# Kernel tuning notes

Hardware: AMD Instinct MI355X
Metric: run time of the kernel (lower is better)

Reference implementation:

```python
import jax, jax.numpy as jnp
import numpy as np

B = 8192          # batch
DEPTH = 2         # variational layers
NCLS = 10         # classes
WIRES = 4         # qubits -> 16-dim statevector
NPATCH = 196      # 14x14 patches of 2x2 on a 28x28 image

# Pauli-Z expectation table: row i = (+1/-1) per wire for basis state i (wire 0 = MSB)
_bits = (np.arange(16)[:, None] >> np.array([3, 2, 1, 0])) & 1
_ZTAB = jnp.asarray(1.0 - 2.0 * _bits, dtype=jnp.float32)  # (16, 4)


def _ry(state, ang, wire):
    # Apply RY(ang) (real rotation) on `wire`; state shape (N,2,2,2,2)
    c = jnp.cos(0.5 * ang)
    s = jnp.sin(0.5 * ang)
    a0 = jnp.take(state, 0, axis=wire + 1)
    a1 = jnp.take(state, 1, axis=wire + 1)
    return jnp.stack([c * a0 - s * a1, s * a0 + c * a1], axis=wire + 1)


def _cnot01(state):  # control wire 0 (axis 1), target wire 1 (axis 2)
    return jnp.stack([state[:, 0], state[:, 1, ::-1]], axis=1)


def _cnot23(state):  # control wire 2 (axis 3), target wire 3 (axis 4)
    return jnp.stack([state[:, :, :, 0], state[:, :, :, 1, ::-1]], axis=3)


def _quanv(patches, theta):
    # patches: (N, 4) pixel angles. Batched 4-qubit statevector simulation.
    half = 0.5 * patches
    v = jnp.stack([jnp.cos(half), jnp.sin(half)], axis=-1)  # (N,4,2): RY(x_w)|0>
    state = jnp.einsum('na,nb,nc,nd->nabcd', v[:, 0], v[:, 1], v[:, 2], v[:, 3])
    for d in range(theta.shape[0]):
        for w in range(WIRES):
            state = _ry(state, theta[d, w], w)
        state = _cnot01(state)
        state = _cnot23(state)
    probs = (state * state).reshape(state.shape[0], 16)
    return probs @ _ZTAB  # (N, 4) <Z_w> expectations


def setup_inputs() -> dict:
    key = jax.random.key(0)
    k1, k2, k3 = jax.random.split(key, 3)
    x = jax.random.normal(k1, (B, 1, 28, 28), dtype=jnp.float32)
    theta = jax.random.normal(k2, (DEPTH, WIRES), dtype=jnp.float32)
    W = jax.random.normal(k3, (NCLS, NPATCH * WIRES), dtype=jnp.float32) * 0.03
    b = jnp.zeros((NCLS,), dtype=jnp.float32)
    return {"x": x, "theta": theta, "W": W, "b": b}


def reference(x, theta, W, b):
    bsz = x.shape[0]
    # extract 2x2 patches in (row-block, col-block) order, pixels row-major
    patches = (x[:, 0]
               .reshape(bsz, 14, 2, 14, 2)
               .transpose(0, 1, 3, 2, 4)
               .reshape(bsz * NPATCH, 4))
    qfeat = _quanv(patches, theta).reshape(bsz, NPATCH * WIRES)  # (B, 784)
    logits = qfeat @ W.T + b
    return jax.nn.log_softmax(logits, axis=-1)
```

## Files before the change

### kernel.cpp

```cpp
#include <hip/hip_runtime.h>
#include <math.h>

#define NP 196
#define NC 10


template<int CTRL>
__device__ __forceinline__ float dpp_add(float v) {
    int t = __builtin_amdgcn_update_dpp(0, __float_as_int(v), CTRL, 0xF, 0xF, true);
    return v + __int_as_float(t);
}

__device__ __forceinline__ float swz_xor16_add(float v) {
    int t = __builtin_amdgcn_ds_swizzle(__float_as_int(v), 0x401F);
    return v + __int_as_float(t);
}

__device__ __forceinline__ void sim_pair(float pxa, float pxb,
                                         float th0a, float th0b,
                                         float ct0, float st0,
                                         float ct1, float st1,
                                         float& z0, float& z1) {
    float sa, ca, sb, cb;
    __sincosf(0.5f * (pxa + th0a), &sa, &ca);
    __sincosf(0.5f * (pxb + th0b), &sb, &cb);
    float p0 = ca * cb, p1 = ca * sb, p2 = sa * sb, p3 = sa * cb;
    float q0 = ct0 * p0 - st0 * p2, q2 = st0 * p0 + ct0 * p2;
    float q1 = ct0 * p1 - st0 * p3, q3 = st0 * p1 + ct0 * p3;
    float r0 = ct1 * q0 - st1 * q1, r1 = st1 * q0 + ct1 * q1;
    float r2 = ct1 * q2 - st1 * q3, r3 = st1 * q2 + ct1 * q3;
    float e0 = r0 * r0, e1 = r1 * r1, e2 = r2 * r2, e3 = r3 * r3;
    z0 = (e0 + e1) - (e2 + e3);
    z1 = (e0 - e1) + (e3 - e2);
}

__global__ __launch_bounds__(256, 2) void quanv_fused(
    const float* __restrict__ x,
    const float* __restrict__ theta,
    const float* __restrict__ W,
    const float* __restrict__ bias,
    float* __restrict__ out,
    int B)
{
    const int tid  = threadIdx.x;
    const int lane = tid & 63;
    const int wave = blockIdx.x * 4 + (tid >> 6);
    const int imgbase = wave * 4;
    if (imgbase >= B) return;

    const float th00 = theta[0], th01 = theta[1], th02 = theta[2], th03 = theta[3];
    float ct[4], st[4];
#pragma unroll
    for (int w = 0; w < 4; ++w) __sincosf(0.5f * theta[4 + w], &st[w], &ct[w]);

    const float* x0 = x + (size_t)imgbase * 784;

    float acc[4][NC];
#pragma unroll
    for (int m = 0; m < 4; ++m)
#pragma unroll
        for (int c = 0; c < NC; ++c) acc[m][c] = 0.f;

#pragma unroll
    for (int k = 0; k < 4; ++k) {
        const bool active = (k < 3) || (lane < 4);
        const int p = lane + 64 * k;
        const int pi = p / 14;
        const int pj = p - pi * 14;
        const int off = pi * 56 + pj * 2;

        float f[4][4];
        if (active) {
#pragma unroll
            for (int m = 0; m < 4; ++m) {
                const float* xm = x0 + m * 784 + off;
                const float2 r0 = *(const float2*)(xm);
                const float2 r1 = *(const float2*)(xm + 28);
                sim_pair(r0.x, r0.y, th00, th01, ct[0], st[0], ct[1], st[1],
                         f[m][0], f[m][1]);
                sim_pair(r1.x, r1.y, th02, th03, ct[2], st[2], ct[3], st[3],
                         f[m][2], f[m][3]);
            }
#pragma unroll
            for (int c = 0; c < NC; ++c) {
                const float4 w4 = *(const float4*)(W + c * 784 + p * 4);
#pragma unroll
                for (int m = 0; m < 4; ++m) {
                    acc[m][c] = fmaf(f[m][0], w4.x, fmaf(f[m][1], w4.y,
                                fmaf(f[m][2], w4.z, fmaf(f[m][3], w4.w, acc[m][c]))));
                }
            }
        }
    }

    const bool lo32 = (lane & 32) == 0;
    const bool lo16 = (lane & 16) == 0;
    float m4[NC];
#pragma unroll
    for (int c = 0; c < NC; ++c) {
        float tAB = lo32 ? acc[0][c] : acc[1][c];
        float uAB = lo32 ? acc[1][c] : acc[0][c];
        float mAB = tAB + __shfl_xor(uAB, 32);
        float tCD = lo32 ? acc[2][c] : acc[3][c];
        float uCD = lo32 ? acc[3][c] : acc[2][c];
        float mCD = tCD + __shfl_xor(uCD, 32);
        float t = lo16 ? mAB : mCD;
        float u = lo16 ? mCD : mAB;
        float v = t + swz_xor16_add(u) - u;
        v = dpp_add<0x124>(v);
        v = dpp_add<0x128>(v);
        v = dpp_add<0xB1>(v);
        v = dpp_add<0x4E>(v);
        m4[c] = v + bias[c];
    }

    float mx = m4[0];
#pragma unroll
    for (int c = 1; c < NC; ++c) mx = fmaxf(mx, m4[c]);
    float se = 0.f;
#pragma unroll
    for (int c = 0; c < NC; ++c) se += __expf(m4[c] - mx);
    const float lse = mx + __logf(se);

    const int r  = lane >> 4;
    const int cl = lane & 15;
    const int img = imgbase + ((r & 1) << 1) + (r >> 1);
    float val = m4[0];
#pragma unroll
    for (int c = 1; c < NC; ++c) val = (cl == c) ? m4[c] : val;
    if (cl < NC) out[img * NC + cl] = val - lse;
}

extern "C" void kernel_launch(void* const* d_in, const int* in_sizes, int n_in,
                              void* d_out, int out_size, void* d_ws, size_t ws_size,
                              hipStream_t stream) {
    const float* x     = (const float*)d_in[0];
    const float* theta = (const float*)d_in[1];
    const float* W     = (const float*)d_in[2];
    const float* bias  = (const float*)d_in[3];
    float* out = (float*)d_out;
    const int B = in_sizes[0] / 784;
    const int waves  = (B + 3) / 4;
    const int blocks = (waves + 3) / 4;
    quanv_fused<<<blocks, 256, 0, stream>>>(x, theta, W, bias, out, B);
}
```

Measured before the change: 15.64 us.

## Split each 4-image group's patches across four waves with LDS cross-wave reduction

Each block now handles 4 images, and each of its 4 waves takes 49 of the 196 patches. Per-wave partial logits are combined through shared memory, and wave 0 computes log-softmax with DPP reductions. This launches four times as many blocks and gives each thread a single patch instead of a 4-iteration loop. The aim is more parallelism and lower register pressure, at the cost of a __syncthreads, an LDS round trip, 15 idle lanes per wave, and W being reloaded by four times as many waves. Launch bounds also rise to 4 blocks per CU.

```diff
diff --git a/kernel.cpp b/kernel.cpp
--- a/kernel.cpp
+++ b/kernel.cpp
@@ -6,14 +6,13 @@
 
 
 template<int CTRL>
-__device__ __forceinline__ float dpp_add(float v) {
-    int t = __builtin_amdgcn_update_dpp(0, __float_as_int(v), CTRL, 0xF, 0xF, true);
-    return v + __int_as_float(t);
+__device__ __forceinline__ float dpp_mov(float v) {
+    return __int_as_float(__builtin_amdgcn_update_dpp(
+        0, __float_as_int(v), CTRL, 0xF, 0xF, true));
 }
 
-__device__ __forceinline__ float swz_xor16_add(float v) {
-    int t = __builtin_amdgcn_ds_swizzle(__float_as_int(v), 0x401F);
-    return v + __int_as_float(t);
+__device__ __forceinline__ float swz_xor16(float v) {
+    return __int_as_float(__builtin_amdgcn_ds_swizzle(__float_as_int(v), 0x401F));
 }
 
 __device__ __forceinline__ void sim_pair(float pxa, float pxb,
@@ -34,7 +33,7 @@
     z1 = (e0 - e1) + (e3 - e2);
 }
 
-__global__ __launch_bounds__(256, 2) void quanv_fused(
+__global__ __launch_bounds__(256, 4) void quanv_fused(
     const float* __restrict__ x,
     const float* __restrict__ theta,
     const float* __restrict__ W,
@@ -42,10 +41,12 @@
     float* __restrict__ out,
     int B)
 {
+    __shared__ float s_part[4][4][16];
+
     const int tid  = threadIdx.x;
     const int lane = tid & 63;
-    const int wave = blockIdx.x * 4 + (tid >> 6);
-    const int imgbase = wave * 4;
+    const int wv   = tid >> 6;
+    const int imgbase = blockIdx.x * 4;
     if (imgbase >= B) return;
 
     const float th00 = theta[0], th01 = theta[1], th02 = theta[2], th03 = theta[3];
@@ -53,49 +54,44 @@
 #pragma unroll
     for (int w = 0; w < 4; ++w) __sincosf(0.5f * theta[4 + w], &st[w], &ct[w]);
 
+    const int   lc    = (lane < 49) ? lane : 48;
+    const int   p     = wv * 49 + lc;
+    const float scale = (lane < 49) ? 1.f : 0.f;
+    const int   pi    = p / 14;
+    const int   pj    = p - pi * 14;
+    const int   off   = pi * 56 + pj * 2;
+
     const float* x0 = x + (size_t)imgbase * 784;
+
+    float f[4][4];
+#pragma unroll
+    for (int m = 0; m < 4; ++m) {
+        const float* xm = x0 + m * 784 + off;
+        const float2 r0 = *(const float2*)(xm);
+        const float2 r1 = *(const float2*)(xm + 28);
+        sim_pair(r0.x, r0.y, th00, th01, ct[0], st[0], ct[1], st[1], f[m][0], f[m][1]);
+        sim_pair(r1.x, r1.y, th02, th03, ct[2], st[2], ct[3], st[3], f[m][2], f[m][3]);
+#pragma unroll
+        for (int j = 0; j < 4; ++j) f[m][j] *= scale;
+    }
 
     float acc[4][NC];
 #pragma unroll
-    for (int m = 0; m < 4; ++m)
+    for (int c = 0; c < NC; ++c) {
+        const float4 w4 = *(const float4*)(W + c * 784 + p * 4);
 #pragma unroll
-        for (int c = 0; c < NC; ++c) acc[m][c] = 0.f;
-
-#pragma unroll
-    for (int k = 0; k < 4; ++k) {
-        const bool active = (k < 3) || (lane < 4);
-        const int p = lane + 64 * k;
-        const int pi = p / 14;
-        const int pj = p - pi * 14;
-        const int off = pi * 56 + pj * 2;
-
-        float f[4][4];
-        if (active) {
-#pragma unroll
-            for (int m = 0; m < 4; ++m) {
-                const float* xm = x0 + m * 784 + off;
-                const float2 r0 = *(const float2*)(xm);
-                const float2 r1 = *(const float2*)(xm + 28);
-                sim_pair(r0.x, r0.y, th00, th01, ct[0], st[0], ct[1], st[1],
-                         f[m][0], f[m][1]);
-                sim_pair(r1.x, r1.y, th02, th03, ct[2], st[2], ct[3], st[3],
-                         f[m][2], f[m][3]);
-            }
-#pragma unroll
-            for (int c = 0; c < NC; ++c) {
-                const float4 w4 = *(const float4*)(W + c * 784 + p * 4);
-#pragma unroll
-                for (int m = 0; m < 4; ++m) {
-                    acc[m][c] = fmaf(f[m][0], w4.x, fmaf(f[m][1], w4.y,
-                                fmaf(f[m][2], w4.z, fmaf(f[m][3], w4.w, acc[m][c]))));
-                }
-            }
+        for (int m = 0; m < 4; ++m) {
+            acc[m][c] = fmaf(f[m][0], w4.x, fmaf(f[m][1], w4.y,
+                        fmaf(f[m][2], w4.z,      f[m][3] * w4.w)));
         }
     }
 
     const bool lo32 = (lane & 32) == 0;
     const bool lo16 = (lane & 16) == 0;
-    float m4[NC];
+    const int  r    = lane >> 4;
+    const int  cl   = lane & 15;
+
+    float val = 0.f;
 #pragma unroll
     for (int c = 0; c < NC; ++c) {
         float tAB = lo32 ? acc[0][c] : acc[1][c];
@@ -106,29 +102,37 @@
         float mCD = tCD + __shfl_xor(uCD, 32);
         float t = lo16 ? mAB : mCD;
         float u = lo16 ? mCD : mAB;
-        float v = t + swz_xor16_add(u) - u;
-        v = dpp_add<0x124>(v);
-        v = dpp_add<0x128>(v);
-        v = dpp_add<0xB1>(v);
-        v = dpp_add<0x4E>(v);
-        m4[c] = v + bias[c];
+        float v = t + swz_xor16(u);
+        v = v + dpp_mov<0x124>(v);
+        v = v + dpp_mov<0x128>(v);
+        v = v + dpp_mov<0xB1>(v);
+        v = v + dpp_mov<0x4E>(v);
+        val = (cl == c) ? v : val;
     }
+    if (cl < NC) s_part[wv][r][cl] = val;
+    __syncthreads();
 
-    float mx = m4[0];
-#pragma unroll
-    for (int c = 1; c < NC; ++c) mx = fmaxf(mx, m4[c]);
-    float se = 0.f;
-#pragma unroll
-    for (int c = 0; c < NC; ++c) se += __expf(m4[c] - mx);
-    const float lse = mx + __logf(se);
+    if (wv == 0) {
+        const int cs = (cl < NC) ? cl : (NC - 1);
+        float lsum = s_part[0][r][cs] + s_part[1][r][cs]
+                   + s_part[2][r][cs] + s_part[3][r][cs] + bias[cs];
+        float logit = (cl < NC) ? lsum : -INFINITY;
 
-    const int r  = lane >> 4;
-    const int cl = lane & 15;
-    const int img = imgbase + ((r & 1) << 1) + (r >> 1);
-    float val = m4[0];
-#pragma unroll
-    for (int c = 1; c < NC; ++c) val = (cl == c) ? m4[c] : val;
-    if (cl < NC) out[img * NC + cl] = val - lse;
+        float mx = logit;
+        mx = fmaxf(mx, dpp_mov<0x124>(mx));
+        mx = fmaxf(mx, dpp_mov<0x128>(mx));
+        mx = fmaxf(mx, dpp_mov<0xB1>(mx));
+        mx = fmaxf(mx, dpp_mov<0x4E>(mx));
+
+        float e = (cl < NC) ? __expf(logit - mx) : 0.f;
+        e = e + dpp_mov<0x124>(e);
+        e = e + dpp_mov<0x128>(e);
+        e = e + dpp_mov<0xB1>(e);
+        e = e + dpp_mov<0x4E>(e);
+
+        const int img = imgbase + ((r & 1) << 1) + (r >> 1);
+        if (cl < NC) out[img * NC + cl] = logit - mx - __logf(e);
+    }
 }
 
 extern "C" void kernel_launch(void* const* d_in, const int* in_sizes, int n_in,
@@ -140,7 +144,6 @@
     const float* bias  = (const float*)d_in[3];
     float* out = (float*)d_out;
     const int B = in_sizes[0] / 784;
-    const int waves  = (B + 3) / 4;
-    const int blocks = (waves + 3) / 4;
+    const int blocks = (B + 3) / 4;
     quanv_fused<<<blocks, 256, 0, stream>>>(x, theta, W, bias, out, B);
 }
```

After: 15.83 us. No clear change (+1.2%).
